# Kernel optimization log

Measured on AMD Instinct MI355X. Metric: run time of the kernel, lower is better.

## Reference

```python
import jax, jax.numpy as jnp
import numpy as np

N_KPTS = 10  # polynomial degree / number of keypoints (E-CIR default)
BS, H, W = 8, 180, 240


def setup_inputs() -> dict:
    key = jax.random.key(0)
    k1, k2, k3 = jax.random.split(key, 3)
    # keypoints ~ evenly spaced timestamps in [-1,1] with small jitter so
    # Lagrange denominators prod_{j!=i}(kp_i - kp_j) are well-conditioned.
    base = jnp.linspace(-1.0, 1.0, N_KPTS, dtype=jnp.float32).reshape(1, N_KPTS, 1, 1)
    keypoints = base + 0.02 * jax.random.normal(k1, (BS, N_KPTS, H, W), dtype=jnp.float32)
    derivative = jax.random.normal(k2, (BS, N_KPTS, H, W), dtype=jnp.float32)
    blurry = jax.random.uniform(k3, (BS, 1, H, W), dtype=jnp.float32)
    return {"derivative": derivative, "blurry": blurry, "keypoints": keypoints}


def _integrator_cache(keypoints):
    # keypoints: (bs, n, h, w) -> cache: (bs, n_deg, n_kpts, h, w)
    # Original computes, for each basis i and order o:
    #   cache[:, o, i] = [sum over (n-1-o)-subsets S of {j!=i} of prod(-kp_j, j in S)]
    #                    / (o+1) / prod_{j!=i}(kp_i - kp_j)
    # The combinatorial sum is exactly the coefficient of x^o in
    # prod_{j!=i}(x - kp_j), so we build it with a polynomial-product
    # recurrence (n-1 fused multiply-adds) instead of 2^(n-1) combination terms.
    bs, n, h, w = keypoints.shape
    rows = []
    for i in range(n):
        others = [j for j in range(n) if j != i]
        denom = jnp.ones((bs, h, w), keypoints.dtype)
        for j in others:
            denom = denom * (keypoints[:, i] - keypoints[:, j])
        # c[o] = coeff of x^o in prod of (x - kp_j) factors processed so far
        c = [jnp.ones((bs, h, w), keypoints.dtype)] + [jnp.zeros((bs, h, w), keypoints.dtype) for _ in range(n - 1)]
        for j in others:
            kp = keypoints[:, j]
            c = [(c[k - 1] - kp * c[k]) if k > 0 else (-kp * c[k]) for k in range(n)]
        inv_denom = 1.0 / denom  # (bs, h, w)
        row = jnp.stack([c[o] * (inv_denom / (o + 1)) for o in range(n)], axis=1)  # (bs, n_deg, h, w)
        rows.append(row)
    return jnp.stack(rows, axis=2)  # (bs, n_deg, n_kpts, h, w)


def reference(derivative, blurry, keypoints):
    # derivative: (bs, n_kpts, h, w); blurry: (bs, 1, h, w); keypoints: (bs, n_kpts, h, w)
    n = keypoints.shape[1]
    integrator_cache = _integrator_cache(keypoints)
    # coeffs[:, o] = sum_i cache[:, o, i] * derivative[:, i]
    coeffs = jnp.einsum('boihw,bihw->bohw', integrator_cache, derivative)
    # integral of polynomial over x in [-1, 1] shifted by x: odd-order terms only
    integral = 2.0 * coeffs[:, 1] / 3.0
    for i in range(3, n, 2):
        integral = integral + 2.0 * coeffs[:, i] / (i + 2)
    baseline = (2.0 * blurry[:, 0] - integral) / 2.0  # (bs, h, w)
    coeffs = jnp.concatenate([baseline[:, None], coeffs], axis=1)  # (bs, n_kpts+1, h, w)
    return coeffs, integrator_cache
```

## Files before the change

### kernel.cpp

```cpp
#include <hip/hip_runtime.h>

#define N_KPTS 10
#define BS 8
#define HH 180
#define WW 240
#define HW (HH * WW)
#define NPIX (BS * HW)
#define NT2 (NPIX / 2)
#define COEFFS_SIZE (BS * (N_KPTS + 1) * HW)

typedef float f32x2 __attribute__((ext_vector_type(2)));

static __device__ __forceinline__ f32x2 splat2(float x) { return (f32x2){x, x}; }
static __device__ __forceinline__ f32x2 vfma2(f32x2 a, f32x2 b, f32x2 c) {
    f32x2 r;
    r.x = fmaf(a.x, b.x, c.x);
    r.y = fmaf(a.y, b.y, c.y);
    return r;
}

__global__ __launch_bounds__(256) void curve_integrator_kernel(
    const float* __restrict__ deriv,
    const float* __restrict__ blurry,
    const float* __restrict__ kpts,
    float* __restrict__ out_coeffs,
    float* __restrict__ out_cache)
{
    int t = blockIdx.x * blockDim.x + threadIdx.x;
    if (t >= NT2) return;
    int p  = t * 2;
    int b  = p / HW;
    int hw = p - b * HW;

    const float* kp_base    = kpts  + (size_t)b * N_KPTS * HW + hw;
    const float* d_base     = deriv + (size_t)b * N_KPTS * HW + hw;
    float*       cache_base = out_cache + (size_t)b * N_KPTS * N_KPTS * HW + hw;

    f32x2 kp[N_KPTS];
#pragma unroll
    for (int i = 0; i < N_KPTS; ++i)
        kp[i] = *(const f32x2*)(kp_base + (size_t)i * HW);

    f32x2 coeffs[N_KPTS];
#pragma unroll
    for (int o = 0; o < N_KPTS; ++o) coeffs[o] = splat2(0.0f);

    const float rcp_tab[N_KPTS] = {
        1.0f, 1.0f/2.0f, 1.0f/3.0f, 1.0f/4.0f, 1.0f/5.0f,
        1.0f/6.0f, 1.0f/7.0f, 1.0f/8.0f, 1.0f/9.0f, 1.0f/10.0f
    };

#pragma unroll
    for (int i = 0; i < N_KPTS; ++i) {
        f32x2 c[N_KPTS];
        c[0] = splat2(1.0f);
#pragma unroll
        for (int k = 1; k < N_KPTS; ++k) c[k] = splat2(0.0f);

        f32x2 denom = splat2(1.0f);
#pragma unroll
        for (int j = 0; j < N_KPTS; ++j) {
            if (j == i) continue;
            f32x2 nkpj = -kp[j];
            denom = denom * (kp[i] - kp[j]);
#pragma unroll
            for (int k = N_KPTS - 1; k >= 1; --k)
                c[k] = vfma2(nkpj, c[k], c[k - 1]);
            c[0] = nkpj * c[0];
        }

        f32x2 inv = splat2(1.0f) / denom;
        f32x2 di  = *(const f32x2*)(d_base + (size_t)i * HW);
#pragma unroll
        for (int o = 0; o < N_KPTS; ++o) {
            f32x2 v = c[o] * (inv * splat2(rcp_tab[o]));
            *(f32x2*)(cache_base + (size_t)(o * N_KPTS + i) * HW) = v;
            coeffs[o] = vfma2(v, di, coeffs[o]);
        }
    }

    f32x2 integral = coeffs[1] * splat2(2.0f / 3.0f);
    integral = vfma2(coeffs[3], splat2(2.0f / 5.0f), integral);
    integral = vfma2(coeffs[5], splat2(2.0f / 7.0f), integral);
    integral = vfma2(coeffs[7], splat2(2.0f / 9.0f), integral);
    integral = vfma2(coeffs[9], splat2(2.0f / 11.0f), integral);

    f32x2 bl = *(const f32x2*)(blurry + (size_t)b * HW + hw);
    f32x2 baseline = (bl * splat2(2.0f) - integral) * splat2(0.5f);

    float* oc = out_coeffs + (size_t)b * (N_KPTS + 1) * HW + hw;
    *(f32x2*)oc = baseline;
#pragma unroll
    for (int o = 0; o < N_KPTS; ++o)
        *(f32x2*)(oc + (size_t)(o + 1) * HW) = coeffs[o];
}

extern "C" void kernel_launch(void* const* d_in, const int* in_sizes, int n_in,
                              void* d_out, int out_size, void* d_ws, size_t ws_size,
                              hipStream_t stream) {
    const float* deriv  = (const float*)d_in[0];
    const float* blurry = (const float*)d_in[1];
    const float* kpts   = (const float*)d_in[2];

    float* out_coeffs = (float*)d_out;
    float* out_cache  = (float*)d_out + COEFFS_SIZE;

    int threads = 256;
    int blocks  = (NT2 + threads - 1) / threads;
    curve_integrator_kernel<<<blocks, threads, 0, stream>>>(
        deriv, blurry, kpts, out_coeffs, out_cache);
}
```

Before: 32.58 us.

## Split each pixel pair's work across two wavefronts by output order halves

Each pixel pair is now handled by two wavefronts. Both recompute the full Lagrange polynomial products, but one writes cache orders 0-4 and coefficients 0-4 plus the baseline, and the other writes orders 5-9. Block count doubles so the grid covers all pixels with twice the threads. This spreads the store-heavy output traffic over more waves to raise parallelism and memory-level concurrency, at the cost of doing the arithmetic and input loads twice.

```diff
diff --git a/kernel.cpp b/kernel.cpp
--- a/kernel.cpp
+++ b/kernel.cpp
@@ -6,7 +6,6 @@
 #define WW 240
 #define HW (HH * WW)
 #define NPIX (BS * HW)
-#define NT2 (NPIX / 2)
 #define COEFFS_SIZE (BS * (N_KPTS + 1) * HW)
 
 typedef float f32x2 __attribute__((ext_vector_type(2)));
@@ -19,19 +18,13 @@
     return r;
 }
 
-__global__ __launch_bounds__(256) void curve_integrator_kernel(
-    const float* __restrict__ deriv,
-    const float* __restrict__ blurry,
-    const float* __restrict__ kpts,
-    float* __restrict__ out_coeffs,
+template <int H>
+static __device__ __forceinline__ void curve_body(
+    int b, int hw,
+    const float* __restrict__ deriv, const float* __restrict__ blurry,
+    const float* __restrict__ kpts, float* __restrict__ out_coeffs,
     float* __restrict__ out_cache)
 {
-    int t = blockIdx.x * blockDim.x + threadIdx.x;
-    if (t >= NT2) return;
-    int p  = t * 2;
-    int b  = p / HW;
-    int hw = p - b * HW;
-
     const float* kp_base    = kpts  + (size_t)b * N_KPTS * HW + hw;
     const float* d_base     = deriv + (size_t)b * N_KPTS * HW + hw;
     float*       cache_base = out_cache + (size_t)b * N_KPTS * N_KPTS * HW + hw;
@@ -74,25 +67,54 @@
 #pragma unroll
         for (int o = 0; o < N_KPTS; ++o) {
             f32x2 v = c[o] * (inv * splat2(rcp_tab[o]));
-            *(f32x2*)(cache_base + (size_t)(o * N_KPTS + i) * HW) = v;
-            coeffs[o] = vfma2(v, di, coeffs[o]);
+            if ((H == 0) ? (o < 5) : (o >= 5))
+                *(f32x2*)(cache_base + (size_t)(o * N_KPTS + i) * HW) = v;
+            if (H == 0 || o >= 5)
+                coeffs[o] = vfma2(v, di, coeffs[o]);
         }
     }
 
-    f32x2 integral = coeffs[1] * splat2(2.0f / 3.0f);
-    integral = vfma2(coeffs[3], splat2(2.0f / 5.0f), integral);
-    integral = vfma2(coeffs[5], splat2(2.0f / 7.0f), integral);
-    integral = vfma2(coeffs[7], splat2(2.0f / 9.0f), integral);
-    integral = vfma2(coeffs[9], splat2(2.0f / 11.0f), integral);
+    float* oc = out_coeffs + (size_t)b * (N_KPTS + 1) * HW + hw;
+    if (H == 0) {
+        f32x2 integral = coeffs[1] * splat2(2.0f / 3.0f);
+        integral = vfma2(coeffs[3], splat2(2.0f / 5.0f), integral);
+        integral = vfma2(coeffs[5], splat2(2.0f / 7.0f), integral);
+        integral = vfma2(coeffs[7], splat2(2.0f / 9.0f), integral);
+        integral = vfma2(coeffs[9], splat2(2.0f / 11.0f), integral);
 
-    f32x2 bl = *(const f32x2*)(blurry + (size_t)b * HW + hw);
-    f32x2 baseline = (bl * splat2(2.0f) - integral) * splat2(0.5f);
+        f32x2 bl = *(const f32x2*)(blurry + (size_t)b * HW + hw);
+        f32x2 baseline = (bl * splat2(2.0f) - integral) * splat2(0.5f);
 
-    float* oc = out_coeffs + (size_t)b * (N_KPTS + 1) * HW + hw;
-    *(f32x2*)oc = baseline;
+        *(f32x2*)oc = baseline;
 #pragma unroll
-    for (int o = 0; o < N_KPTS; ++o)
-        *(f32x2*)(oc + (size_t)(o + 1) * HW) = coeffs[o];
+        for (int o = 0; o < 5; ++o)
+            *(f32x2*)(oc + (size_t)(o + 1) * HW) = coeffs[o];
+    } else {
+#pragma unroll
+        for (int o = 5; o < N_KPTS; ++o)
+            *(f32x2*)(oc + (size_t)(o + 1) * HW) = coeffs[o];
+    }
+}
+
+__global__ __launch_bounds__(256) void curve_integrator_kernel(
+    const float* __restrict__ deriv,
+    const float* __restrict__ blurry,
+    const float* __restrict__ kpts,
+    float* __restrict__ out_coeffs,
+    float* __restrict__ out_cache)
+{
+    const int lane = threadIdx.x & 63;
+    const int w    = threadIdx.x >> 6;
+    const int h    = w >> 1;
+    const int pr   = blockIdx.x * 128 + ((w & 1) << 6) + lane;
+    const int p    = pr * 2;
+    const int b    = p / HW;
+    const int hw   = p - b * HW;
+
+    if (h == 0)
+        curve_body<0>(b, hw, deriv, blurry, kpts, out_coeffs, out_cache);
+    else
+        curve_body<1>(b, hw, deriv, blurry, kpts, out_coeffs, out_cache);
 }
 
 extern "C" void kernel_launch(void* const* d_in, const int* in_sizes, int n_in,
@@ -106,7 +128,7 @@
     float* out_cache  = (float*)d_out + COEFFS_SIZE;
 
     int threads = 256;
-    int blocks  = (NT2 + threads - 1) / threads;
+    int blocks  = NPIX / threads;
     curve_integrator_kernel<<<blocks, threads, 0, stream>>>(
         deriv, blurry, kpts, out_coeffs, out_cache);
 }
```

Result: slower. 34.99 us (+7.4%).
